# Kernel tuning notes

Measured on AMD Instinct MI355X. Metric: run time of the kernel, lower is better.

Reference implementation:

```python
import jax, jax.numpy as jnp
import numpy as np

B, H, W, D, C = 1, 32, 32, 32, 256
WS = (8, 8, 8)
SS = (4, 4, 4)
NH = 8
HD = C // NH
N = WS[0] * WS[1] * WS[2]
NW = (H // WS[0]) * (W // WS[1]) * (D // WS[2])


def _rel_pos_index():
    coords = np.stack(np.meshgrid(np.arange(WS[0]), np.arange(WS[1]), np.arange(WS[2]), indexing='ij'))
    cf = coords.reshape(3, -1)
    rc = (cf[:, :, None] - cf[:, None, :]).transpose(1, 2, 0).astype(np.int64)
    rc[:, :, 0] += WS[0] - 1
    rc[:, :, 1] += WS[1] - 1
    rc[:, :, 2] += WS[2] - 1
    rc[:, :, 0] *= (2 * WS[2] - 1) * (2 * WS[1] - 1)
    rc[:, :, 1] *= (2 * WS[2] - 1)
    return rc.sum(-1).reshape(-1)  # [N*N]


def _attn_mask():
    m = np.zeros((H, W, D), np.float32)
    cnt = 0

    def sl(ws, ss):
        return ((0, -ws), (-ws, -ss), (-ss, None))

    for hs in sl(WS[0], SS[0]):
        for ws_ in sl(WS[1], SS[1]):
            for ds in sl(WS[2], SS[2]):
                m[hs[0]:hs[1], ws_[0]:ws_[1], ds[0]:ds[1]] = cnt
                cnt += 1
    m = m.reshape(H // WS[0], WS[0], W // WS[1], WS[1], D // WS[2], WS[2])
    m = m.transpose(0, 2, 4, 1, 3, 5).reshape(NW, N)
    diff = m[:, None, :] - m[:, :, None]  # [NW, N, N]
    return np.where(diff != 0, -100.0, 0.0).astype(np.float32)


REL_IDX = jnp.asarray(_rel_pos_index())
ATTN_MASK = jnp.asarray(_attn_mask())  # [NW, N, N]


def setup_inputs() -> dict:
    key = jax.random.key(0)
    ks = jax.random.split(key, 4)
    return {
        'x': jax.random.normal(ks[0], (B, H, W, D, C), jnp.float32),
        'qkv_weight': jax.random.normal(ks[1], (3 * C, C), jnp.float32) * 0.02,
        'qkv_bias': jnp.zeros((3 * C,), jnp.float32),
        'proj_weight': jax.random.normal(ks[2], (C, C), jnp.float32) * 0.02,
        'proj_bias': jnp.zeros((C,), jnp.float32),
        'rpb_table': jax.random.normal(ks[3], ((2 * WS[0] - 1) * (2 * WS[1] - 1) * (2 * WS[2] - 1), NH), jnp.float32) * 0.02,
    }


def reference(x, qkv_weight, qkv_bias, proj_weight, proj_bias, rpb_table):
    # cyclic shift
    xs = jnp.roll(x, (-SS[0], -SS[1], -SS[2]), axis=(1, 2, 3))
    # window partition -> [B*NW, N, C]
    xw = xs.reshape(B, H // WS[0], WS[0], W // WS[1], WS[1], D // WS[2], WS[2], C)
    xw = xw.transpose(0, 1, 3, 5, 2, 4, 6, 7).reshape(B * NW, N, C)
    # qkv projection
    qkv = xw @ qkv_weight.T + qkv_bias
    qkv = qkv.reshape(B * NW, N, 3, NH, HD).transpose(2, 0, 3, 1, 4)  # [3, B*NW, NH, N, HD]
    q, k, v = qkv[0] * (HD ** -0.5), qkv[1], qkv[2]
    # relative position bias [NH, N, N]
    bias = rpb_table[REL_IDX].reshape(N, N, NH).transpose(2, 0, 1)
    attn = jnp.einsum('whnd,whmd->whnm', q, k) + bias[None]
    # shift mask per window
    attn = attn.reshape(B, NW, NH, N, N) + ATTN_MASK[None, :, None]
    attn = jax.nn.softmax(attn.reshape(B * NW, NH, N, N), axis=-1)
    out = jnp.einsum('whnm,whmd->whnd', attn, v)
    out = out.transpose(0, 2, 1, 3).reshape(B * NW, N, C)
    out = out @ proj_weight.T + proj_bias
    # un-window -> [B, H, W, D, C]
    out = out.reshape(B, H // WS[0], W // WS[1], D // WS[2], WS[0], WS[1], WS[2], C)
    out = out.transpose(0, 1, 4, 2, 5, 3, 6, 7).reshape(B, H, W, D, C)
    # reverse cyclic shift
    return jnp.roll(out, (SS[0], SS[1], SS[2]), axis=(1, 2, 3))
```

## Files before the change

### kernel.cpp

```cpp
#include <hip/hip_runtime.h>

typedef __attribute__((ext_vector_type(8))) short short8;
typedef __attribute__((ext_vector_type(4))) short s4v;
typedef __attribute__((ext_vector_type(2))) uint uint2v;
typedef __attribute__((ext_vector_type(4))) float floatx4;

#define CCH   256
#define QSCALE 0.17677669529663687f

__device__ __forceinline__ unsigned short f2bf(float f) {
    unsigned u = __float_as_uint(f);
    u = u + 0x7fffu + ((u >> 16) & 1u);
    return (unsigned short)(u >> 16);
}

__device__ __forceinline__ void gl_lds16(const void* g, void* l) {
    __builtin_amdgcn_global_load_lds((const __attribute__((address_space(1))) void*)g,
                                     (__attribute__((address_space(3))) void*)l, 16, 0, 0);
}

__device__ __forceinline__ int spatial_off(int token) {
    int w = token >> 9, n = token & 511;
    int wh = w >> 4, ww = (w >> 2) & 3, wd = w & 3;
    int h1 = n >> 6, w1 = (n >> 3) & 7, d1 = n & 7;
    int gh = (wh * 8 + h1 + 4) & 31;
    int gw = (ww * 8 + w1 + 4) & 31;
    int gd = (wd * 8 + d1 + 4) & 31;
    return ((gh * 32 + gw) * 32 + gd) * CCH;
}

__global__ __launch_bounds__(256) void xconv(const float* __restrict__ x,
                                             ushort* __restrict__ Xw) {
    int tid = blockIdx.x * 256 + threadIdx.x;
    int token = tid >> 5, c8 = (tid & 31) * 8;
    const float* src = x + spatial_off(token) + c8;
    float4 a = *(const float4*)src;
    float4 b = *(const float4*)(src + 4);
    uint2v lo, hi;
    lo[0] = (uint)f2bf(a.x) | ((uint)f2bf(a.y) << 16);
    lo[1] = (uint)f2bf(a.z) | ((uint)f2bf(a.w) << 16);
    hi[0] = (uint)f2bf(b.x) | ((uint)f2bf(b.y) << 16);
    hi[1] = (uint)f2bf(b.z) | ((uint)f2bf(b.w) << 16);
    uint2v* dst = (uint2v*)(Xw + (size_t)token * 256 + c8);
    dst[0] = lo;
    dst[1] = hi;
}

__global__ __launch_bounds__(256) void wconv(const float* __restrict__ Wq,
                                             const float* __restrict__ Wp,
                                             ushort* __restrict__ Wqb,
                                             ushort* __restrict__ Wpb) {
    int tid = blockIdx.x * 256 + threadIdx.x;
    if (tid < 196608) {
        float s = (tid < 65536) ? QSCALE : 1.0f;
        Wqb[tid] = f2bf(Wq[tid] * s);
    } else {
        int i = tid - 196608;
        Wpb[i] = f2bf(Wp[i]);
    }
}

__global__ __launch_bounds__(256) void pair_prep(const float* __restrict__ rpb,
                                                 uint* __restrict__ Up) {
    int tid = blockIdx.x * 256 + threadIdx.x;
    if (tid >= 27000) return;
    int head = tid / 3375, idx = tid - head * 3375;
    uint lo = f2bf(rpb[idx * 8 + head]);
    uint hi = f2bf(rpb[(idx > 0 ? idx - 1 : 0) * 8 + head]);
    Up[tid] = lo | (hi << 16);
}

__global__ __launch_bounds__(256) void gemm_qkv(
    const ushort* __restrict__ A,
    const ushort* __restrict__ Bw,
    const float* __restrict__ bq,
    ushort* __restrict__ Q, ushort* __restrict__ K, ushort* __restrict__ Vf) {
    __shared__ short As[128 * 64];
    __shared__ short Bs[128 * 64];
    const int t = threadIdx.x;
    const int wv = t >> 6, lane = t & 63, quad = lane >> 4, col = lane & 15;
    const int m0 = blockIdx.y * 128, n0 = blockIdx.x * 128;
    const int wm = (wv & 1) * 64, wn = (wv >> 1) * 64;

    floatx4 zf = {0.f, 0.f, 0.f, 0.f};
    floatx4 acc[4][4];
#pragma unroll
    for (int i = 0; i < 4; ++i)
#pragma unroll
        for (int j = 0; j < 4; ++j) acc[i][j] = zf;

    for (int kk = 0; kk < 256; kk += 64) {
        __syncthreads();
#pragma unroll
        for (int i = 0; i < 4; ++i) {
            int s = i * 256 + t;
            int row = s >> 3, qs = s & 7;
            int qg = qs ^ (row & 7);
            gl_lds16(A + (size_t)(m0 + row) * 256 + kk + qg * 8,
                     As + (i * 256 + wv * 64) * 8);
        }
#pragma unroll
        for (int i = 0; i < 4; ++i) {
            int s = i * 256 + t;
            int row = s >> 3, qs = s & 7;
            int qg = qs ^ (row & 7);
            gl_lds16(Bw + (size_t)(n0 + row) * 256 + kk + qg * 8,
                     Bs + (i * 256 + wv * 64) * 8);
        }
        __syncthreads();
#pragma unroll
        for (int h = 0; h < 2; ++h) {
            short8 af[4], bf[4];
#pragma unroll
            for (int mi = 0; mi < 4; ++mi) {
                int row = wm + mi * 16 + col;
                af[mi] = *(const short8*)(As + (row * 8 + ((h * 4 + quad) ^ (row & 7))) * 8);
            }
#pragma unroll
            for (int ni = 0; ni < 4; ++ni) {
                int row = wn + ni * 16 + col;
                bf[ni] = *(const short8*)(Bs + (row * 8 + ((h * 4 + quad) ^ (row & 7))) * 8);
            }
#pragma unroll
            for (int mi = 0; mi < 4; ++mi)
#pragma unroll
                for (int ni = 0; ni < 4; ++ni)
                    acc[mi][ni] = __builtin_amdgcn_mfma_f32_16x16x32_bf16(af[mi], bf[ni], acc[mi][ni], 0, 0, 0);
        }
    }

#pragma unroll
    for (int ni = 0; ni < 4; ++ni) {
        int j = n0 + wn + ni * 16 + col;
        int three = j >> 8, head = (j >> 5) & 7, hd = j & 31;
        float bias = bq[j] * ((j < 256) ? QSCALE : 1.0f);
        if (three == 2) {
            int h = hd >> 4, colv = hd & 15;
#pragma unroll
            for (int mi = 0; mi < 4; ++mi) {
#pragma unroll
                for (int r = 0; r < 4; ++r) {
                    int m = m0 + wm + mi * 16 + quad * 4 + r;
                    int w = m >> 9, n = m & 511;
                    size_t off = ((size_t)((w * 8 + head) * 64 + (n >> 4) * 2 + h) << 8)
                               + ((((n >> 2) & 3) * 16 + colv) << 2) + (n & 3);
                    Vf[off] = f2bf(acc[mi][ni][r] + bias);
                }
            }
        } else {
            ushort* dst = (three == 0) ? Q : K;
#pragma unroll
            for (int mi = 0; mi < 4; ++mi) {
#pragma unroll
                for (int r = 0; r < 4; ++r) {
                    int m = m0 + wm + mi * 16 + quad * 4 + r;
                    int w = m >> 9, n = m & 511;
                    dst[((size_t)(w * 8 + head) * 512 + n) * 32 + hd] = f2bf(acc[mi][ni][r] + bias);
                }
            }
        }
    }
}

__global__ __launch_bounds__(256) void gemm_proj(
    const ushort* __restrict__ A,
    const ushort* __restrict__ Bw,
    const float* __restrict__ bp,
    float* __restrict__ out) {
    __shared__ short As[128 * 64];
    __shared__ short Bs[128 * 64];
    const int t = threadIdx.x;
    const int wv = t >> 6, lane = t & 63, quad = lane >> 4, col = lane & 15;
    const int m0 = blockIdx.y * 128, n0 = blockIdx.x * 128;
    const int wm = (wv & 1) * 64, wn = (wv >> 1) * 64;

    floatx4 zf = {0.f, 0.f, 0.f, 0.f};
    floatx4 acc[4][4];
#pragma unroll
    for (int i = 0; i < 4; ++i)
#pragma unroll
        for (int j = 0; j < 4; ++j) acc[i][j] = zf;

    for (int kk = 0; kk < 256; kk += 64) {
        __syncthreads();
#pragma unroll
        for (int i = 0; i < 4; ++i) {
            int s = i * 256 + t;
            int row = s >> 3, qs = s & 7;
            int qg = qs ^ (row & 7);
            gl_lds16(A + (size_t)(m0 + row) * 256 + kk + qg * 8,
                     As + (i * 256 + wv * 64) * 8);
        }
#pragma unroll
        for (int i = 0; i < 4; ++i) {
            int s = i * 256 + t;
            int row = s >> 3, qs = s & 7;
            int qg = qs ^ (row & 7);
            gl_lds16(Bw + (size_t)(n0 + row) * 256 + kk + qg * 8,
                     Bs + (i * 256 + wv * 64) * 8);
        }
        __syncthreads();
#pragma unroll
        for (int h = 0; h < 2; ++h) {
            short8 af[4], bf[4];
#pragma unroll
            for (int mi = 0; mi < 4; ++mi) {
                int row = wm + mi * 16 + col;
                af[mi] = *(const short8*)(As + (row * 8 + ((h * 4 + quad) ^ (row & 7))) * 8);
            }
#pragma unroll
            for (int ni = 0; ni < 4; ++ni) {
                int row = wn + ni * 16 + col;
                bf[ni] = *(const short8*)(Bs + (row * 8 + ((h * 4 + quad) ^ (row & 7))) * 8);
            }
#pragma unroll
            for (int mi = 0; mi < 4; ++mi)
#pragma unroll
                for (int ni = 0; ni < 4; ++ni)
                    acc[mi][ni] = __builtin_amdgcn_mfma_f32_16x16x32_bf16(af[mi], bf[ni], acc[mi][ni], 0, 0, 0);
        }
    }

#pragma unroll
    for (int ni = 0; ni < 4; ++ni) {
        int j = n0 + wn + ni * 16 + col;
        float bias = bp[j];
#pragma unroll
        for (int mi = 0; mi < 4; ++mi) {
#pragma unroll
            for (int r = 0; r < 4; ++r) {
                int m = m0 + wm + mi * 16 + quad * 4 + r;
                out[spatial_off(m) + j] = acc[mi][ni][r] + bias;
            }
        }
    }
}

__global__ __launch_bounds__(256, 2) void attn_kernel(
    const ushort* __restrict__ Q, const ushort* __restrict__ K,
    const ushort* __restrict__ Vf, const uint* __restrict__ Up,
    ushort* __restrict__ Y) {
    __shared__ short Kl[512 * 32];
    __shared__ short Vs[64 * 256];
    __shared__ uint  Ul[3375];

    const int t = threadIdx.x;
    const int bid = blockIdx.x;
    const int w = bid >> 3, head = bid & 7;
    const int wh = w >> 4, ww = (w >> 2) & 3, wd = w & 3;
    const int wv = t >> 6, lane = t & 63, quad = lane >> 4, col = lane & 15;

    const ushort* Kg = K + (size_t)(w * 8 + head) * 512 * 32;
    const ushort* Vg = Vf + (size_t)(w * 8 + head) * 512 * 32;
    const ushort* Qg = Q + (size_t)(w * 8 + head) * 512 * 32;

#pragma unroll
    for (int i = 0; i < 8; ++i) {
        gl_lds16(Kg + (size_t)(i * 256 + t) * 8, Kl + (i * 256 + wv * 64) * 8);
        gl_lds16(Vg + (size_t)(i * 256 + t) * 8, Vs + (i * 256 + wv * 64) * 8);
    }
    const uint* Uph = Up + head * 3375;
    for (int i = t; i < 3375; i += 256) Ul[i] = Uph[i];
    __syncthreads();

    const bool boundary = (wh == 3) | (ww == 3) | (wd == 3);
    floatx4 zf = {0.f, 0.f, 0.f, 0.f};

    for (int qs = 0; qs < 8; ++qs) {
        const int qt = wv * 8 + qs;
        const short8 qf = *(const short8*)(Qg + (size_t)(qt * 16 + col) * 32 + quad * 8);

        const int qrow = qt * 16 + col;
        const int qh = qrow >> 6, qw = (qrow >> 3) & 7, qd = qrow & 7;
        const int Base0 = ((qh + 7) * 15 + (qw + 7 - (quad >> 1))) * 15
                        + (qd - ((quad & 1) << 2) + 7);
        const int cq = ((wh == 3) ? (1 + ((qrow >> 8) & 1)) * 16 : 0)
                     + ((ww == 3) ? (1 + ((qrow >> 5) & 1)) * 4 : 0)
                     + ((wd == 3) ? (1 + ((qrow >> 2) & 1)) : 0);

        float rs = 0.f;
        floatx4 o0 = zf, o1 = zf;

        for (int c = 0; c < 2; ++c) {
            const short* KlC = Kl + c * 8192;
            const short* VsC = Vs + c * 8192;
            const int BaseC = Base0 - c * 900;
            const int ckh = (wh == 3) ? ((1 + c) * 16) : 0;

            floatx4 acc[16];
#pragma unroll
            for (int tt = 0; tt < 16; ++tt) {
                short8 kf = *(const short8*)(KlC + tt * 512 + col * 32 + quad * 8);
                acc[tt] = __builtin_amdgcn_mfma_f32_16x16x32_bf16(kf, qf, zf, 0, 0, 0);
            }

#pragma unroll
            for (int tt = 0; tt < 16; ++tt) {
                const int Kt2 = ((tt >> 2) * 15 + (tt & 3) * 2) * 15;
                uint p0 = Ul[BaseC - Kt2];
                uint p1 = Ul[BaseC - Kt2 - 2];
                float s0 = acc[tt][0] + __uint_as_float(p0 << 16);
                float s1 = acc[tt][1] + __uint_as_float(p0 & 0xffff0000u);
                float s2 = acc[tt][2] + __uint_as_float(p1 << 16);
                float s3 = acc[tt][3] + __uint_as_float(p1 & 0xffff0000u);
                if (boundary) {
                    int ck = ckh
                           + ((ww == 3) ? (1 + ((tt >> 1) & 1)) * 4 : 0)
                           + ((wd == 3) ? (1 + (quad & 1)) : 0);
                    float madd = (cq == ck) ? 0.f : -100.f;
                    s0 += madd; s1 += madd; s2 += madd; s3 += madd;
                }
                float e0 = exp2f(s0 * 1.442695041f);
                float e1 = exp2f(s1 * 1.442695041f);
                float e2 = exp2f(s2 * 1.442695041f);
                float e3 = exp2f(s3 * 1.442695041f);
                rs += (e0 + e1) + (e2 + e3);
                uint2v pp;
                pp[0] = (uint)f2bf(e0) | ((uint)f2bf(e1) << 16);
                pp[1] = (uint)f2bf(e2) | ((uint)f2bf(e3) << 16);
                s4v pf = __builtin_bit_cast(s4v, pp);
                s4v v0 = *(const s4v*)(VsC + ((tt * 2 + 0) << 8) + lane * 4);
                s4v v1 = *(const s4v*)(VsC + ((tt * 2 + 1) << 8) + lane * 4);
                o0 = __builtin_amdgcn_mfma_f32_16x16x16bf16_1k(v0, pf, o0, 0, 0, 0);
                o1 = __builtin_amdgcn_mfma_f32_16x16x16bf16_1k(v1, pf, o1, 0, 0, 0);
            }
        }

        rs += __shfl_xor(rs, 16);
        rs += __shfl_xor(rs, 32);
        const float inv = 1.0f / rs;

        int token = w * 512 + qt * 16 + col;
        ushort* Yb = Y + (size_t)token * 256 + head * 32 + quad * 4;
        uint2v y0, y1;
        y0[0] = (uint)f2bf(o0[0] * inv) | ((uint)f2bf(o0[1] * inv) << 16);
        y0[1] = (uint)f2bf(o0[2] * inv) | ((uint)f2bf(o0[3] * inv) << 16);
        y1[0] = (uint)f2bf(o1[0] * inv) | ((uint)f2bf(o1[1] * inv) << 16);
        y1[1] = (uint)f2bf(o1[2] * inv) | ((uint)f2bf(o1[3] * inv) << 16);
        *(uint2v*)(Yb) = y0;
        *(uint2v*)(Yb + 16) = y1;
    }
}

extern "C" void kernel_launch(void* const* d_in, const int* in_sizes, int n_in,
                              void* d_out, int out_size, void* d_ws, size_t ws_size,
                              hipStream_t stream) {
    const float* x      = (const float*)d_in[0];
    const float* qkv_w  = (const float*)d_in[1];
    const float* qkv_b  = (const float*)d_in[2];
    const float* proj_w = (const float*)d_in[3];
    const float* proj_b = (const float*)d_in[4];
    const float* rpb    = (const float*)d_in[5];
    float* out = (float*)d_out;

    ushort* Xw  = (ushort*)d_ws;
    ushort* Q   = Xw + 8388608;
    ushort* K   = Q + 8388608;
    ushort* Vf  = K + 8388608;
    ushort* Y   = Vf + 8388608;
    uint*   Up  = (uint*)(Y + 8388608);
    ushort* Wqb = (ushort*)(Up + 27008);
    ushort* Wpb = Wqb + 196608;

    xconv<<<dim3(4096), dim3(256), 0, stream>>>(x, Xw);
    wconv<<<dim3(1024), dim3(256), 0, stream>>>(qkv_w, proj_w, Wqb, Wpb);
    pair_prep<<<dim3(106), dim3(256), 0, stream>>>(rpb, Up);
    gemm_qkv<<<dim3(6, 256), dim3(256), 0, stream>>>(Xw, Wqb, qkv_b, Q, K, Vf);
    attn_kernel<<<dim3(512), dim3(256), 0, stream>>>(Q, K, Vf, Up, Y);
    gemm_proj<<<dim3(2, 256), dim3(256), 0, stream>>>(Y, Wpb, proj_b, out);
}
```

Baseline: 209.7 us.

## Fold log2e into Q scale and bias, inject bias via MFMA accumulator

Pre-multiplies the Q weights, Q bias and relative-position table by log2(e) so the softmax can call exp2 directly without a per-element multiply. The bias and mask are loaded into the MFMA accumulator input instead of being added afterwards. It also packs bf16 conversions with a round-half-up byte-perm helper, writes V as vectorized 8-byte stores, and uses a hardware reciprocal. Rounding changes slightly: there is no ties-to-even handling, and rcp is approximate.

```diff
diff --git a/kernel.cpp b/kernel.cpp
--- a/kernel.cpp
+++ b/kernel.cpp
@@ -7,11 +7,18 @@
 
 #define CCH   256
 #define QSCALE 0.17677669529663687f
+#define LOG2E  1.4426950408889634f
 
 __device__ __forceinline__ unsigned short f2bf(float f) {
     unsigned u = __float_as_uint(f);
     u = u + 0x7fffu + ((u >> 16) & 1u);
     return (unsigned short)(u >> 16);
+}
+
+__device__ __forceinline__ uint pk2bf(float a, float b) {
+    uint ua = __float_as_uint(a) + 0x8000u;
+    uint ub = __float_as_uint(b) + 0x8000u;
+    return __builtin_amdgcn_perm(ub, ua, 0x07060302u);
 }
 
 __device__ __forceinline__ void gl_lds16(const void* g, void* l) {
@@ -37,10 +44,10 @@
     float4 a = *(const float4*)src;
     float4 b = *(const float4*)(src + 4);
     uint2v lo, hi;
-    lo[0] = (uint)f2bf(a.x) | ((uint)f2bf(a.y) << 16);
-    lo[1] = (uint)f2bf(a.z) | ((uint)f2bf(a.w) << 16);
-    hi[0] = (uint)f2bf(b.x) | ((uint)f2bf(b.y) << 16);
-    hi[1] = (uint)f2bf(b.z) | ((uint)f2bf(b.w) << 16);
+    lo[0] = pk2bf(a.x, a.y);
+    lo[1] = pk2bf(a.z, a.w);
+    hi[0] = pk2bf(b.x, b.y);
+    hi[1] = pk2bf(b.z, b.w);
     uint2v* dst = (uint2v*)(Xw + (size_t)token * 256 + c8);
     dst[0] = lo;
     dst[1] = hi;
@@ -52,7 +59,7 @@
                                              ushort* __restrict__ Wpb) {
     int tid = blockIdx.x * 256 + threadIdx.x;
     if (tid < 196608) {
-        float s = (tid < 65536) ? QSCALE : 1.0f;
+        float s = (tid < 65536) ? (QSCALE * LOG2E) : 1.0f;
         Wqb[tid] = f2bf(Wq[tid] * s);
     } else {
         int i = tid - 196608;
@@ -65,8 +72,8 @@
     int tid = blockIdx.x * 256 + threadIdx.x;
     if (tid >= 27000) return;
     int head = tid / 3375, idx = tid - head * 3375;
-    uint lo = f2bf(rpb[idx * 8 + head]);
-    uint hi = f2bf(rpb[(idx > 0 ? idx - 1 : 0) * 8 + head]);
+    uint lo = f2bf(rpb[idx * 8 + head] * LOG2E);
+    uint hi = f2bf(rpb[(idx > 0 ? idx - 1 : 0) * 8 + head] * LOG2E);
     Up[tid] = lo | (hi << 16);
 }
 
@@ -133,19 +140,19 @@
     for (int ni = 0; ni < 4; ++ni) {
         int j = n0 + wn + ni * 16 + col;
         int three = j >> 8, head = (j >> 5) & 7, hd = j & 31;
-        float bias = bq[j] * ((j < 256) ? QSCALE : 1.0f);
+        float bias = bq[j] * ((j < 256) ? (QSCALE * LOG2E) : 1.0f);
         if (three == 2) {
             int h = hd >> 4, colv = hd & 15;
 #pragma unroll
             for (int mi = 0; mi < 4; ++mi) {
-#pragma unroll
-                for (int r = 0; r < 4; ++r) {
-                    int m = m0 + wm + mi * 16 + quad * 4 + r;
-                    int w = m >> 9, n = m & 511;
-                    size_t off = ((size_t)((w * 8 + head) * 64 + (n >> 4) * 2 + h) << 8)
-                               + ((((n >> 2) & 3) * 16 + colv) << 2) + (n & 3);
-                    Vf[off] = f2bf(acc[mi][ni][r] + bias);
-                }
+                int mb = m0 + wm + mi * 16 + quad * 4;
+                int w = mb >> 9, n = mb & 511;
+                size_t off = ((size_t)((w * 8 + head) * 64 + (n >> 4) * 2 + h) << 8)
+                           + ((((n >> 2) & 3) * 16 + colv) << 2);
+                uint2v pv;
+                pv[0] = pk2bf(acc[mi][ni][0] + bias, acc[mi][ni][1] + bias);
+                pv[1] = pk2bf(acc[mi][ni][2] + bias, acc[mi][ni][3] + bias);
+                *(uint2v*)(Vf + off) = pv;
             }
         } else {
             ushort* dst = (three == 0) ? Q : K;
@@ -290,34 +297,35 @@
             floatx4 acc[16];
 #pragma unroll
             for (int tt = 0; tt < 16; ++tt) {
-                short8 kf = *(const short8*)(KlC + tt * 512 + col * 32 + quad * 8);
-                acc[tt] = __builtin_amdgcn_mfma_f32_16x16x32_bf16(kf, qf, zf, 0, 0, 0);
-            }
-
-#pragma unroll
-            for (int tt = 0; tt < 16; ++tt) {
                 const int Kt2 = ((tt >> 2) * 15 + (tt & 3) * 2) * 15;
                 uint p0 = Ul[BaseC - Kt2];
                 uint p1 = Ul[BaseC - Kt2 - 2];
-                float s0 = acc[tt][0] + __uint_as_float(p0 << 16);
-                float s1 = acc[tt][1] + __uint_as_float(p0 & 0xffff0000u);
-                float s2 = acc[tt][2] + __uint_as_float(p1 << 16);
-                float s3 = acc[tt][3] + __uint_as_float(p1 & 0xffff0000u);
+                floatx4 cf;
+                cf[0] = __uint_as_float(p0 << 16);
+                cf[1] = __uint_as_float(p0 & 0xffff0000u);
+                cf[2] = __uint_as_float(p1 << 16);
+                cf[3] = __uint_as_float(p1 & 0xffff0000u);
                 if (boundary) {
                     int ck = ckh
                            + ((ww == 3) ? (1 + ((tt >> 1) & 1)) * 4 : 0)
                            + ((wd == 3) ? (1 + (quad & 1)) : 0);
-                    float madd = (cq == ck) ? 0.f : -100.f;
-                    s0 += madd; s1 += madd; s2 += madd; s3 += madd;
+                    float madd = (cq == ck) ? 0.f : -144.269504f;
+                    cf[0] += madd; cf[1] += madd; cf[2] += madd; cf[3] += madd;
                 }
-                float e0 = exp2f(s0 * 1.442695041f);
-                float e1 = exp2f(s1 * 1.442695041f);
-                float e2 = exp2f(s2 * 1.442695041f);
-                float e3 = exp2f(s3 * 1.442695041f);
+                short8 kf = *(const short8*)(KlC + tt * 512 + col * 32 + quad * 8);
+                acc[tt] = __builtin_amdgcn_mfma_f32_16x16x32_bf16(kf, qf, cf, 0, 0, 0);
+            }
+
+#pragma unroll
+            for (int tt = 0; tt < 16; ++tt) {
+                float e0 = exp2f(acc[tt][0]);
+                float e1 = exp2f(acc[tt][1]);
+                float e2 = exp2f(acc[tt][2]);
+                float e3 = exp2f(acc[tt][3]);
                 rs += (e0 + e1) + (e2 + e3);
                 uint2v pp;
-                pp[0] = (uint)f2bf(e0) | ((uint)f2bf(e1) << 16);
-                pp[1] = (uint)f2bf(e2) | ((uint)f2bf(e3) << 16);
+                pp[0] = pk2bf(e0, e1);
+                pp[1] = pk2bf(e2, e3);
                 s4v pf = __builtin_bit_cast(s4v, pp);
                 s4v v0 = *(const s4v*)(VsC + ((tt * 2 + 0) << 8) + lane * 4);
                 s4v v1 = *(const s4v*)(VsC + ((tt * 2 + 1) << 8) + lane * 4);
@@ -328,15 +336,15 @@
 
         rs += __shfl_xor(rs, 16);
         rs += __shfl_xor(rs, 32);
-        const float inv = 1.0f / rs;
+        const float inv = __builtin_amdgcn_rcpf(rs);
 
         int token = w * 512 + qt * 16 + col;
         ushort* Yb = Y + (size_t)token * 256 + head * 32 + quad * 4;
         uint2v y0, y1;
-        y0[0] = (uint)f2bf(o0[0] * inv) | ((uint)f2bf(o0[1] * inv) << 16);
-        y0[1] = (uint)f2bf(o0[2] * inv) | ((uint)f2bf(o0[3] * inv) << 16);
-        y1[0] = (uint)f2bf(o1[0] * inv) | ((uint)f2bf(o1[1] * inv) << 16);
-        y1[1] = (uint)f2bf(o1[2] * inv) | ((uint)f2bf(o1[3] * inv) << 16);
+        y0[0] = pk2bf(o0[0] * inv, o0[1] * inv);
+        y0[1] = pk2bf(o0[2] * inv, o0[3] * inv);
+        y1[0] = pk2bf(o1[0] * inv, o1[1] * inv);
+        y1[1] = pk2bf(o1[2] * inv, o1[3] * inv);
         *(uint2v*)(Yb) = y0;
         *(uint2v*)(Yb + 16) = y1;
     }
```

Result: faster. 200.9 us (-4.2%).
